# Kernel tuning notes

Measured on AMD Instinct MI355X. Metric: run time of the kernel, lower is better.

The kernel has to match this reference:

```python
import jax, jax.numpy as jnp
import numpy as np

T, A, E, RAW, H, NACT, NTP = 64, 48, 22, 512, 256, 21, 3
# entity_distinct: self entity [0], friendly entities [1:12], hostile entities [12:22]
PARAM_SHAPES = [
    ("W1", (NTP, RAW, H)), ("b1", (NTP, H)), ("W2", (NTP, H, H)), ("b2", (NTP, H)),
    ("WCf", (NTP, 2 * H, H)), ("bCf", (NTP, H)), ("WMf", (NTP, 2 * H + 2 * RAW, H)), ("bMf", (NTP, H)),
    ("WCh", (NTP, 2 * H, H)), ("bCh", (NTP, H)), ("WMh", (NTP, 2 * H + 2 * RAW, H)), ("bMh", (NTP, H)),
    ("L1", (NTP, 2 * H, H)), ("bL1", (NTP, H)), ("L2", (NTP, H, H // 2)), ("bL2", (NTP, H // 2)),
    ("L3", (NTP, H // 2, NACT)), ("bL3", (NTP, NACT)),
    ("V1", (NTP, 2 * H, H)), ("bV1", (NTP, H)), ("V2", (NTP, H, 1)), ("bV2", (NTP, 1)),
]
PNAMES = [n for n, _ in PARAM_SHAPES]


def setup_inputs() -> dict:
    key = jax.random.key(0)
    ks = jax.random.split(key, 3 + len(PARAM_SHAPES))
    inp = {
        "obs": jax.random.normal(ks[0], (T, A, E, RAW), jnp.float32),
        "hete_pick": jax.random.randint(ks[1], (T, A), 0, NTP, jnp.int32),
        "dead": jax.random.bernoulli(ks[2], 0.15, (T, A, E)),
    }
    for i, (n, s) in enumerate(PARAM_SHAPES):
        inp[n] = jax.random.normal(ks[3 + i], s, jnp.float32) * 0.02
    return inp


def _net_forward(p, obs, dead):
    relu = jax.nn.relu
    obs = jnp.where(dead[..., None], 0.0, obs)                    # nan_to_num for dead entities
    v = relu(obs @ p["W1"] + p["b1"]) @ p["W2"] + p["b2"]         # [T,A,E,H] per-entity encoder
    zs, ze_f, ze_h = obs[..., 0, :], obs[..., 1:12, :], obs[..., 12:22, :]
    vs, ve_f, ve_h = v[..., 0, :], v[..., 1:12, :], v[..., 12:22, :]
    df, dh = dead[..., 1:12], dead[..., 12:22]

    def conc(ve, d, ze, WC, bC, WM, bM):
        w = (~d).astype(obs.dtype)                                # alive mask [T,A,Ef]
        denom = jnp.maximum(w.sum(-1, keepdims=True), 1.0)
        pool = jnp.einsum('taeh,tae->tah', ve, w) / denom         # masked mean over entities
        pool_z = jnp.einsum('taer,tae->tar', ze, w) / denom       # skip-connect raw-obs pool
        vC = relu(jnp.concatenate([vs, pool], -1) @ WC + bC)
        vM = relu(jnp.concatenate([vs, pool, zs, pool_z], -1) @ WM + bM)
        return vC, vM

    vfC, vfM = conc(ve_f, df, ze_f, p["WCf"], p["bCf"], p["WMf"], p["bMf"])
    vhC, vhM = conc(ve_h, dh, ze_h, p["WCh"], p["bCh"], p["WMh"], p["bMh"])
    vC = jnp.concatenate([vfC, vhC], -1)                          # [T,A,2H] dual-conc fuse
    vM = jnp.concatenate([vfM, vhM], -1)
    logits = relu(relu(vC @ p["L1"] + p["bL1"]) @ p["L2"] + p["bL2"]) @ p["L3"] + p["bL3"]
    value = relu(vM @ p["V1"] + p["bV1"]) @ p["V2"] + p["bV2"]    # [T,A,1]
    logp = jax.nn.log_softmax(logits, -1)
    act = jnp.argmax(logits, -1)                                  # deterministic (test_mode) action
    alp = jnp.take_along_axis(logp, act[..., None], -1)           # [T,A,1] action log-prob
    return act, value, alp


def reference(obs, hete_pick, dead, W1, b1, W2, b2, WCf, bCf, WMf, bMf, WCh, bCh, WMh, bMh,
              L1, bL1, L2, bL2, L3, bL3, V1, bV1, V2, bV2):
    params = dict(W1=W1, b1=b1, W2=W2, b2=b2, WCf=WCf, bCf=bCf, WMf=WMf, bMf=bMf,
                  WCh=WCh, bCh=bCh, WMh=WMh, bMh=bMh, L1=L1, bL1=bL1, L2=L2, bL2=bL2,
                  L3=L3, bL3=bL3, V1=V1, bV1=bV1, V2=V2, bV2=bV2)
    act = jnp.zeros((T, A), jnp.int32)
    value = jnp.zeros((T, A, 1), obs.dtype)
    alp = jnp.zeros((T, A, 1), obs.dtype)
    for t in range(NTP):                                          # heterogeneous dispatch (distribute_compute)
        pt = {k: v[t] for k, v in params.items()}
        a_t, v_t, lp_t = _net_forward(pt, obs, dead)
        m = hete_pick == t                                        # mask_arr[t]
        act = jnp.where(m, a_t.astype(jnp.int32), act)
        value = jnp.where(m[..., None], v_t, value)
        alp = jnp.where(m[..., None], lp_t, alp)
    return act, value, alp
```

## Files before the change

kernel.cpp:

```cpp
#include <hip/hip_runtime.h>
#include <cstdint>

#define T_ 64
#define A_ 48
#define NP_ 3072
#define E_ 22
#define RAW_ 512
#define H_ 256
#define NACT_ 21
#define NTP_ 3
#define PV_ 3456
#define RV_ 68096
#define NDEAD_ 67584

typedef unsigned short u16;
typedef __attribute__((ext_vector_type(8))) short short8;
typedef __attribute__((ext_vector_type(4))) short short4v;
typedef __attribute__((ext_vector_type(4))) float floatx4;

__device__ __forceinline__ u16 f2bf(float x) {
    unsigned r;
    asm("v_cvt_pk_bf16_f32 %0, %1, %1" : "=v"(r) : "v"(x));
    return (u16)r;
}
__device__ __forceinline__ float bf2f(u16 h) {
    return __uint_as_float(((unsigned)h) << 16);
}

typedef __attribute__((address_space(1))) const void* gp_t;
typedef __attribute__((address_space(3))) void* lp_t;
__device__ __forceinline__ void gload16(const void* g, void* l) {
    __builtin_amdgcn_global_load_lds((gp_t)g, (lp_t)l, 16, 0, 0);
}

__global__ void k_bucket(const unsigned* __restrict__ deadRaw,
                         const int* __restrict__ hete, int* __restrict__ wsI)
{
    __shared__ int fl[2];
    __shared__ int sc[3], cur[3], sps[3], srs[3];
    int tid = threadIdx.x;
    if (tid < 2) fl[tid] = 0;
    if (tid < 3) { sc[tid] = 0; cur[tid] = 0; }
    __syncthreads();
    int ni = 0, nf = 0;
    for (int i = tid; i < 1024; i += 256) {
        unsigned w = deadRaw[i];
        if (w > 1u) ni = 1;
        if (w != 0u && w != 0x3F800000u) nf = 1;
    }
    if (ni) atomicOr(&fl[0], 1);
    if (nf) atomicOr(&fl[1], 1);
    for (int p = tid; p < NP_; p += 256) atomicAdd(&sc[hete[p]], 1);
    __syncthreads();
    if (tid == 0) {
        int c0 = sc[0], c1 = sc[1], c2 = sc[2];
        int p1 = (c0 + 127) & ~127;
        int p2 = p1 + ((c1 + 127) & ~127);
        sps[0] = 0; sps[1] = p1; sps[2] = p2;
        int r1 = (22 * c0 + 127) & ~127;
        int r2 = r1 + ((22 * c1 + 127) & ~127);
        srs[0] = 0; srs[1] = r1; srs[2] = r2;
        wsI[0] = fl[0] ? (fl[1] ? 2 : 1) : 0;
        wsI[1] = c0; wsI[2] = c1; wsI[3] = c2;
        wsI[4] = 0; wsI[5] = p1; wsI[6] = p2;
        wsI[8] = 0; wsI[9] = r1; wsI[10] = r2;
    }
    __syncthreads();
    int* pairIdx = wsI + 16;
    int* prb = pairIdx + PV_;
    for (int pv = tid; pv < PV_; pv += 256) pairIdx[pv] = -1;
    __syncthreads();
    for (int p = tid; p < NP_; p += 256) {
        int t = hete[p];
        int pos = atomicAdd(&cur[t], 1);
        pairIdx[sps[t] + pos] = p;
    }
    for (int pv = tid; pv < PV_; pv += 256) {
        int t = (pv >= sps[1]) + (pv >= sps[2]);
        prb[pv] = srs[t] + 22 * (pv - sps[t]);
    }
}

__global__ void k_deadmask(const void* __restrict__ dead,
                           const int* __restrict__ wsI, float* __restrict__ dm)
{
    int i = blockIdx.x * 256 + threadIdx.x;
    if (i >= NDEAD_) return;
    int mode = wsI[0];
    bool d;
    if (mode == 0)      d = ((const int*)dead)[i] != 0;
    else if (mode == 1) d = ((const float*)dead)[i] != 0.f;
    else                d = ((const unsigned char*)dead)[i] != 0;
    dm[i] = d ? 0.f : 1.f;
}

__global__ void k_rowobs(const int* __restrict__ cnt, const int* __restrict__ ps,
                         const int* __restrict__ rs, const int* __restrict__ pairIdx,
                         const float* __restrict__ dm, int* __restrict__ rowObs)
{
    int rv = blockIdx.x * 256 + threadIdx.x;
    if (rv >= RV_) return;
    int t = (rv >= rs[1]) + (rv >= rs[2]);
    int local = rv - rs[t];
    int out = -1;
    if (local < 22 * cnt[t]) {
        int pl = local / 22;
        int e = local - pl * 22;
        int p = pairIdx[ps[t] + pl];
        if (p >= 0) {
            int oi = p * 22 + e;
            if (dm[oi] != 0.f) out = oi;
        }
    }
    rowObs[rv] = out;
}

struct WCA {
    const float* W[8]; u16* Hi[8]; u16* Lo[8]; int K[8]; int bs[9];
};
__global__ __launch_bounds__(256) void k_wconv(WCA a)
{
    int blk = blockIdx.x;
    int s = 0;
#pragma unroll
    for (int i = 1; i < 8; ++i) if (blk >= a.bs[i]) s = i;
    int lb = blk - a.bs[s];
    int K = a.K[s];
    int K8 = K >> 3;
    int kc = lb % K8;
    int t  = lb / K8;
    int n  = threadIdx.x;
    const float* w = a.W[s] + (long)t * K * 256 + n;
    short8 hv, lv;
#pragma unroll
    for (int j = 0; j < 8; ++j) {
        float x = w[(long)(kc * 8 + j) * 256];
        u16 hh = f2bf(x);
        hv[j] = (short)hh;
        lv[j] = (short)f2bf(x - bf2f(hh));
    }
    long o = ((long)t * 256 + n) * K + kc * 8;
    *(short8*)(a.Hi[s] + o) = hv;
    *(short8*)(a.Lo[s] + o) = lv;
}

struct GD {
    const void* Aa; const void* Ab;
    const u16* Bh; const u16* Bl;
    const float* bias;
    void* Ca; void* Cb;
    long lda; long ldc;
    int K; int coff;
};
struct GA4 { GD d[4]; };

template<int AMODE, bool RELU, int OUTS>
__global__ __launch_bounds__(256) void k_mgemm(
    GA4 ga, const int* __restrict__ rowIdx, const int* __restrict__ starts)
{
    __shared__ short Ah[128 * 32], Al[128 * 32], Bh[128 * 32], Bl[128 * 32];
    const int tid = threadIdx.x;
    const GD d = ga.d[blockIdx.z];
    const long rb = (long)blockIdx.x * 128;
    const int n0 = blockIdx.y * 128;
    const int t = (rb >= starts[0]) + (rb >= starts[1]);
    const int K = d.K;
    const long lda = d.lda;
    const u16* bhT = d.Bh + ((long)t * 256 + n0) * K;
    const u16* blT = d.Bl + ((long)t * 256 + n0) * K;
    const float* biasT = d.bias + (long)t * 256 + n0;

    const int cs = tid & 3;

    const int ar = tid >> 3;
    const int ac = (tid & 7) * 4;
    long arow[4]; float amask[4];
    const float* Afp = (const float*)d.Aa;
    if (AMODE == 1) {
#pragma unroll
        for (int it = 0; it < 4; ++it) {
            int r = 32 * it + ar;
            int i0 = rowIdx[rb + r];
            amask[it] = (i0 < 0) ? 0.f : 1.f;
            arow[it] = (i0 < 0) ? 0 : (long)i0 * lda;
        }
    }
    const u16* ahT = (const u16*)d.Aa;
    const u16* alT = (const u16*)d.Ab;

    const int wave = tid >> 6;
    const int lane = tid & 63;
    const int wr = (wave >> 1) * 64;
    const int wc = (wave & 1) * 64;
    const int lm = lane & 15;
    const int quad = lane >> 4;

    floatx4 acc[4][4];
#pragma unroll
    for (int i = 0; i < 4; ++i)
#pragma unroll
        for (int j = 0; j < 4; ++j) acc[i][j] = (floatx4){0.f, 0.f, 0.f, 0.f};

    for (int k0 = 0; k0 < K; k0 += 32) {
        float4 av[4];
        if (AMODE == 1) {
#pragma unroll
            for (int it = 0; it < 4; ++it)
                av[it] = *(const float4*)(Afp + arow[it] + k0 + ac);
        }
        __syncthreads();
#pragma unroll
        for (int i = 0; i < 2; ++i) {
            int c = i * 256 + tid;
            int r = c >> 2;
            long go = (long)r * K + k0 + ((cs ^ (r & 3)) << 3);
            gload16(bhT + go, &Bh[c << 3]);
            gload16(blT + go, &Bl[c << 3]);
        }
        if (AMODE == 0) {
#pragma unroll
            for (int i = 0; i < 2; ++i) {
                int c = i * 256 + tid;
                int r = c >> 2;
                long go = (rb + r) * lda + k0 + ((cs ^ (r & 3)) << 3);
                gload16(ahT + go, &Ah[c << 3]);
                gload16(alT + go, &Al[c << 3]);
            }
        } else {
#pragma unroll
            for (int it = 0; it < 4; ++it) {
                float xs[4] = {av[it].x, av[it].y, av[it].z, av[it].w};
                short4v hv, lv;
#pragma unroll
                for (int e = 0; e < 4; ++e) {
                    float x = xs[e] * amask[it];
                    u16 hh = f2bf(x);
                    hv[e] = (short)hh;
                    lv[e] = (short)f2bf(x - bf2f(hh));
                }
                int r = 32 * it + ar;
                int bs = ((((ac >> 3) ^ (r & 3))) << 4) | ((ac & 4) << 1);
                *(short4v*)((char*)Ah + r * 64 + bs) = hv;
                *(short4v*)((char*)Al + r * 64 + bs) = lv;
            }
        }
        __syncthreads();
        short8 fah[4], fal[4];
#pragma unroll
        for (int i = 0; i < 4; ++i) {
            int m = wr + 16 * i + lm;
            int sl = (quad ^ (m & 3)) << 3;
            fah[i] = *(const short8*)&Ah[(m << 5) + sl];
            fal[i] = *(const short8*)&Al[(m << 5) + sl];
        }
#pragma unroll
        for (int j = 0; j < 4; ++j) {
            int n = wc + 16 * j + lm;
            int sl = (quad ^ (n & 3)) << 3;
            short8 fbh = *(const short8*)&Bh[(n << 5) + sl];
            short8 fbl = *(const short8*)&Bl[(n << 5) + sl];
#pragma unroll
            for (int i = 0; i < 4; ++i) {
                acc[i][j] = __builtin_amdgcn_mfma_f32_16x16x32_bf16(fah[i], fbh, acc[i][j], 0, 0, 0);
                acc[i][j] = __builtin_amdgcn_mfma_f32_16x16x32_bf16(fal[i], fbh, acc[i][j], 0, 0, 0);
                acc[i][j] = __builtin_amdgcn_mfma_f32_16x16x32_bf16(fah[i], fbl, acc[i][j], 0, 0, 0);
            }
        }
    }
#pragma unroll
    for (int j = 0; j < 4; ++j) {
        int col = wc + 16 * j + lm;
        float bj = biasT[col];
#pragma unroll
        for (int i = 0; i < 4; ++i) {
            long rbase = rb + wr + 16 * i + quad * 4;
#pragma unroll
            for (int r = 0; r < 4; ++r) {
                float vv = acc[i][j][r] + bj;
                if (RELU) vv = fmaxf(vv, 0.f);
                long off = (rbase + r) * d.ldc + d.coff + n0 + col;
                if (OUTS == 0) {
                    ((float*)d.Ca)[off] = vv;
                } else {
                    u16 hh = f2bf(vv);
                    ((u16*)d.Ca)[off] = hh;
                    ((u16*)d.Cb)[off] = f2bf(vv - bf2f(hh));
                }
            }
        }
    }
}

__global__ __launch_bounds__(256) void k_prep(
    const int* __restrict__ pairIdx, const int* __restrict__ prb,
    const float* __restrict__ dm, const float* __restrict__ v,
    const float* __restrict__ obs,
    u16* __restrict__ XFh, u16* __restrict__ XFl,
    u16* __restrict__ XHh, u16* __restrict__ XHl)
{
    int pv = blockIdx.x, c = threadIdx.x;
    int p = pairIdx[pv];
    long xo = (long)pv * 1536;
    if (p < 0) {
        for (int s = 0; s < 6; ++s) {
            XFh[xo + s * 256 + c] = 0; XFl[xo + s * 256 + c] = 0;
            XHh[xo + s * 256 + c] = 0; XHl[xo + s * 256 + c] = 0;
        }
        return;
    }
    __shared__ float sw[22];
    if (c < 22) sw[c] = dm[p * 22 + c];
    __syncthreads();
    float denf = 0.f, denh = 0.f;
    for (int e = 1; e < 12; ++e)  denf += sw[e];
    for (int e = 12; e < 22; ++e) denh += sw[e];
    denf = 1.f / fmaxf(denf, 1.f);
    denh = 1.f / fmaxf(denh, 1.f);

    auto wsp = [&](u16* Hh, u16* Hl, long idx, float val) {
        u16 hh = f2bf(val);
        Hh[idx] = hh;
        Hl[idx] = f2bf(val - bf2f(hh));
    };

    long base = prb[pv];
    float vs = v[base * 256 + c];
    wsp(XFh, XFl, xo + c, vs);
    wsp(XHh, XHl, xo + c, vs);
    float af = 0.f, ah = 0.f;
    for (int e = 1; e < 12; ++e)  af += sw[e] * v[(base + e) * 256 + c];
    for (int e = 12; e < 22; ++e) ah += sw[e] * v[(base + e) * 256 + c];
    wsp(XFh, XFl, xo + 256 + c, af * denf);
    wsp(XHh, XHl, xo + 256 + c, ah * denh);
    const float* ob = obs + (long)p * 22 * 512;
    float w0 = sw[0];
    float z0 = ob[c] * w0;
    float z1 = ob[256 + c] * w0;
    wsp(XFh, XFl, xo + 512 + c, z0); wsp(XHh, XHl, xo + 512 + c, z0);
    wsp(XFh, XFl, xo + 768 + c, z1); wsp(XHh, XHl, xo + 768 + c, z1);
#pragma unroll
    for (int half = 0; half < 2; ++half) {
        int c2 = c + half * 256;
        float zf = 0.f, zh = 0.f;
        for (int e = 1; e < 12; ++e)  zf += sw[e] * ob[(long)e * 512 + c2];
        for (int e = 12; e < 22; ++e) zh += sw[e] * ob[(long)e * 512 + c2];
        wsp(XFh, XFl, xo + 1024 + c2, zf * denf);
        wsp(XHh, XHl, xo + 1024 + c2, zh * denh);
    }
}

__global__ __launch_bounds__(128) void k_final(
    const float* __restrict__ g1, const float* __restrict__ vV,
    const float* __restrict__ L2, const float* __restrict__ bL2,
    const float* __restrict__ L3, const float* __restrict__ bL3,
    const float* __restrict__ V2, const float* __restrict__ bV2,
    const int* __restrict__ pairIdx, const int* __restrict__ ps,
    float* __restrict__ out)
{
    int pv = blockIdx.x;
    int p = pairIdx[pv];
    if (p < 0) return;
    int c = threadIdx.x;
    int t = (pv >= ps[1]) + (pv >= ps[2]);

    __shared__ float sg1[256], sg2[128], sval[2];
    const float* g1p = g1 + (long)pv * 256;
    sg1[c] = g1p[c];
    sg1[c + 128] = g1p[c + 128];

    const float* vv = vV + (long)pv * 256;
    const float* v2t = V2 + t * 256;
    float s = vv[c] * v2t[c] + vv[c + 128] * v2t[c + 128];
    for (int off = 32; off; off >>= 1) s += __shfl_down(s, off);
    if ((c & 63) == 0) sval[c >> 6] = s;
    __syncthreads();

    const float* l2 = L2 + (long)t * 256 * 128 + c;
    float a = bL2[t * 128 + c];
#pragma unroll 8
    for (int k = 0; k < 256; ++k) a = fmaf(sg1[k], l2[(long)k * 128], a);
    sg2[c] = fmaxf(a, 0.f);
    __syncthreads();

    if (c < 64) {
        float lg = -3.0e38f;
        if (c < 21) {
            const float* l3t = L3 + (long)t * 128 * 21 + c;
            float acc = bL3[t * 21 + c];
            for (int k = 0; k < 128; ++k) acc = fmaf(sg2[k], l3t[k * 21], acc);
            lg = acc;
        }
        float mv = lg; int mi = (c < 21) ? c : 9999;
        for (int off = 32; off; off >>= 1) {
            float ov = __shfl_down(mv, off);
            int oi = __shfl_down(mi, off);
            if (ov > mv || (ov == mv && oi < mi)) { mv = ov; mi = oi; }
        }
        mv = __shfl(mv, 0); mi = __shfl(mi, 0);
        float e = (c < 21) ? expf(lg - mv) : 0.f;
        for (int off = 32; off; off >>= 1) e += __shfl_down(e, off);
        if (c == 0) {
            out[p] = (float)mi;
            out[NP_ + p] = sval[0] + sval[1] + bV2[t];
            out[2 * NP_ + p] = -logf(e);
        }
    }
}

extern "C" void kernel_launch(void* const* d_in, const int* in_sizes, int n_in,
                              void* d_out, int out_size, void* d_ws, size_t ws_size,
                              hipStream_t stream)
{
    const float* obs = (const float*)d_in[0];
    const int* hete = (const int*)d_in[1];
    const void* dead = d_in[2];
    const float* W1 = (const float*)d_in[3];  const float* b1 = (const float*)d_in[4];
    const float* W2 = (const float*)d_in[5];  const float* b2 = (const float*)d_in[6];
    const float* WCf = (const float*)d_in[7]; const float* bCf = (const float*)d_in[8];
    const float* WMf = (const float*)d_in[9]; const float* bMf = (const float*)d_in[10];
    const float* WCh = (const float*)d_in[11]; const float* bCh = (const float*)d_in[12];
    const float* WMh = (const float*)d_in[13]; const float* bMh = (const float*)d_in[14];
    const float* L1 = (const float*)d_in[15]; const float* bL1 = (const float*)d_in[16];
    const float* L2 = (const float*)d_in[17]; const float* bL2 = (const float*)d_in[18];
    const float* L3 = (const float*)d_in[19]; const float* bL3 = (const float*)d_in[20];
    const float* V1 = (const float*)d_in[21]; const float* bV1 = (const float*)d_in[22];
    const float* V2 = (const float*)d_in[23]; const float* bV2 = (const float*)d_in[24];
    float* out = (float*)d_out;

    int* wsI = (int*)d_ws;
    int* pairIdx = wsI + 16;
    int* prb = pairIdx + PV_;
    int* rowObs = prb + PV_;
    long fbase = ((16L + PV_ + PV_ + RV_) + 63) & ~63L;
    float* wsF = (float*)d_ws;
    float* dm = wsF + fbase;
    float* cur = dm + NDEAD_;
    auto allocUS = [&](long K) { u16* p = (u16*)cur; cur += (3L * 256 * K) / 2; return p; };
    u16* W1h = allocUS(512);  u16* W1l = allocUS(512);
    u16* W2h = allocUS(256);  u16* W2l = allocUS(256);
    u16* WCfh = allocUS(512); u16* WCfl = allocUS(512);
    u16* WChh = allocUS(512); u16* WChl = allocUS(512);
    u16* WMfh = allocUS(1536); u16* WMfl = allocUS(1536);
    u16* WMhh = allocUS(1536); u16* WMhl = allocUS(1536);
    u16* L1h = allocUS(512);  u16* L1l = allocUS(512);
    u16* V1h = allocUS(512);  u16* V1l = allocUS(512);
    float* regA = cur;
    float* regB = regA + (long)RV_ * 256;

    u16* h1h = (u16*)regA;
    u16* h1l = h1h + (long)RV_ * 256;
    u16* XFh = (u16*)regA;
    u16* XFl = XFh + (long)PV_ * 1536;
    u16* XHh = XFl + (long)PV_ * 1536;
    u16* XHl = XHh + (long)PV_ * 1536;
    float* v = regB;
    u16* vCh = (u16*)regB;
    u16* vCl = vCh + (long)PV_ * 512;
    u16* vMh = vCl + (long)PV_ * 512;
    u16* vMl = vMh + (long)PV_ * 512;
    float* g1 = (float*)(vMl + (long)PV_ * 512);
    float* vV = g1 + (long)PV_ * 256;

    k_bucket<<<1, 256, 0, stream>>>((const unsigned*)dead, hete, wsI);
    k_deadmask<<<264, 256, 0, stream>>>(dead, wsI, dm);
    k_rowobs<<<266, 256, 0, stream>>>(wsI + 1, wsI + 4, wsI + 8, pairIdx, dm, rowObs);

    {
        WCA wa;
        const float* Ws[8] = {W1, W2, WCf, WCh, WMf, WMh, L1, V1};
        u16* His[8] = {W1h, W2h, WCfh, WChh, WMfh, WMhh, L1h, V1h};
        u16* Los[8] = {W1l, W2l, WCfl, WChl, WMfl, WMhl, L1l, V1l};
        int Ks[8] = {512, 256, 512, 512, 1536, 1536, 512, 512};
        int acc_b = 0; wa.bs[0] = 0;
        for (int i = 0; i < 8; ++i) {
            wa.W[i] = Ws[i]; wa.Hi[i] = His[i]; wa.Lo[i] = Los[i]; wa.K[i] = Ks[i];
            acc_b += 3 * Ks[i] / 8; wa.bs[i + 1] = acc_b;
        }
        k_wconv<<<acc_b, 256, 0, stream>>>(wa);
    }

    GA4 g;
    auto setd = [&](int i, const void* Aa, const void* Ab, const u16* Bh_, const u16* Bl_,
                    const float* bias, void* Ca, void* Cb, long lda_, long ldc_, int K_, int coff_) {
        g.d[i] = GD{Aa, Ab, Bh_, Bl_, bias, Ca, Cb, lda_, ldc_, K_, coff_};
    };

    for (int i = 0; i < 4; ++i)
        setd(i, obs, nullptr, W1h, W1l, b1, h1h, h1l, 512, 256, 512, 0);
    k_mgemm<1, true, 1><<<dim3(RV_ / 128, 2, 1), 256, 0, stream>>>(g, rowObs, wsI + 9);

    for (int i = 0; i < 4; ++i)
        setd(i, h1h, h1l, W2h, W2l, b2, v, nullptr, 256, 256, 256, 0);
    k_mgemm<0, false, 0><<<dim3(RV_ / 128, 2, 1), 256, 0, stream>>>(g, nullptr, wsI + 9);

    k_prep<<<PV_, 256, 0, stream>>>(pairIdx, prb, dm, v, obs, XFh, XFl, XHh, XHl);

    setd(0, XFh, XFl, WCfh, WCfl, bCf, vCh, vCl, 1536, 512, 512, 0);
    setd(1, XHh, XHl, WChh, WChl, bCh, vCh, vCl, 1536, 512, 512, 256);
    setd(2, XFh, XFl, WMfh, WMfl, bMf, vMh, vMl, 1536, 512, 1536, 0);
    setd(3, XHh, XHl, WMhh, WMhl, bMh, vMh, vMl, 1536, 512, 1536, 256);
    k_mgemm<0, true, 1><<<dim3(PV_ / 128, 2, 4), 256, 0, stream>>>(g, nullptr, wsI + 5);

    setd(0, vCh, vCl, L1h, L1l, bL1, g1, nullptr, 512, 256, 512, 0);
    setd(1, vMh, vMl, V1h, V1l, bV1, vV, nullptr, 512, 256, 512, 0);
    setd(2, vCh, vCl, L1h, L1l, bL1, g1, nullptr, 512, 256, 512, 0);
    setd(3, vCh, vCl, L1h, L1l, bL1, g1, nullptr, 512, 256, 512, 0);
    k_mgemm<0, true, 0><<<dim3(PV_ / 128, 2, 2), 256, 0, stream>>>(g, nullptr, wsI + 5);

    k_final<<<PV_, 128, 0, stream>>>(g1, vV, L2, bL2, L3, bL3, V2, bV2,
                                     pairIdx, wsI + 4, out);
    (void)in_sizes; (void)n_in; (void)out_size; (void)ws_size;
}
```

Before: 565.2 us.

## Double-buffer GEMM LDS tiles, change swizzle, stage bf16 outputs through LDS

Splits the shared-memory tiles of the split-bf16 grouped GEMM into two buffers. The next K-tile's global-to-LDS loads (and, in the gather mode, its fp32 loads) are issued before the current tile's MFMAs run, so each step needs one barrier instead of two and load latency overlaps compute. The LDS swizzle becomes an XOR of the row bits to cut bank conflicts. The hi/lo bf16 epilogue now writes through LDS so global stores are coalesced 16-byte vectors. LDS use doubles to 64 KB per block, which may lower occupancy.

Measured after the change: 520.3 us. -7.9%, faster.

```diff
diff --git a/kernel.cpp b/kernel.cpp
--- a/kernel.cpp
+++ b/kernel.cpp
@@ -32,6 +32,14 @@
 __device__ __forceinline__ void gload16(const void* g, void* l) {
     __builtin_amdgcn_global_load_lds((gp_t)g, (lp_t)l, 16, 0, 0);
 }
+
+__device__ __forceinline__ void sync_tile() {
+    asm volatile("s_waitcnt vmcnt(0) lgkmcnt(0)" ::: "memory");
+    __builtin_amdgcn_s_barrier();
+    __builtin_amdgcn_sched_barrier(0);
+}
+
+__device__ __forceinline__ int swzk(int r) { return ((r >> 1) ^ r) & 3; }
 
 __global__ void k_bucket(const unsigned* __restrict__ deadRaw,
                          const int* __restrict__ hete, int* __restrict__ wsI)
@@ -158,7 +166,7 @@
 __global__ __launch_bounds__(256) void k_mgemm(
     GA4 ga, const int* __restrict__ rowIdx, const int* __restrict__ starts)
 {
-    __shared__ short Ah[128 * 32], Al[128 * 32], Bh[128 * 32], Bl[128 * 32];
+    __shared__ short smem[32768];
     const int tid = threadIdx.x;
     const GD d = ga.d[blockIdx.z];
     const long rb = (long)blockIdx.x * 128;
@@ -195,68 +203,102 @@
     const int lm = lane & 15;
     const int quad = lane >> 4;
 
-    floatx4 acc[4][4];
-#pragma unroll
-    for (int i = 0; i < 4; ++i)
-#pragma unroll
-        for (int j = 0; j < 4; ++j) acc[i][j] = (floatx4){0.f, 0.f, 0.f, 0.f};
-
-    for (int k0 = 0; k0 < K; k0 += 32) {
-        float4 av[4];
-        if (AMODE == 1) {
-#pragma unroll
-            for (int it = 0; it < 4; ++it)
-                av[it] = *(const float4*)(Afp + arow[it] + k0 + ac);
-        }
-        __syncthreads();
+    auto stageB = [&](int b, int k0) {
+        short* Bh = smem + b * 16384 + 8192;
+        short* Bl = smem + b * 16384 + 12288;
 #pragma unroll
         for (int i = 0; i < 2; ++i) {
             int c = i * 256 + tid;
             int r = c >> 2;
-            long go = (long)r * K + k0 + ((cs ^ (r & 3)) << 3);
+            long go = (long)r * K + k0 + ((cs ^ swzk(r)) << 3);
             gload16(bhT + go, &Bh[c << 3]);
             gload16(blT + go, &Bl[c << 3]);
         }
-        if (AMODE == 0) {
-#pragma unroll
-            for (int i = 0; i < 2; ++i) {
-                int c = i * 256 + tid;
-                int r = c >> 2;
-                long go = (rb + r) * lda + k0 + ((cs ^ (r & 3)) << 3);
-                gload16(ahT + go, &Ah[c << 3]);
-                gload16(alT + go, &Al[c << 3]);
+    };
+    auto stageA0 = [&](int b, int k0) {
+        short* Ah = smem + b * 16384;
+        short* Al = smem + b * 16384 + 4096;
+#pragma unroll
+        for (int i = 0; i < 2; ++i) {
+            int c = i * 256 + tid;
+            int r = c >> 2;
+            long go = (rb + r) * lda + k0 + ((cs ^ swzk(r)) << 3);
+            gload16(ahT + go, &Ah[c << 3]);
+            gload16(alT + go, &Al[c << 3]);
+        }
+    };
+    auto convertA = [&](int b, const float4* av) {
+        short* AhW = smem + b * 16384;
+        short* AlW = AhW + 4096;
+#pragma unroll
+        for (int it = 0; it < 4; ++it) {
+            float xs[4] = {av[it].x, av[it].y, av[it].z, av[it].w};
+            short4v hv, lv;
+#pragma unroll
+            for (int e = 0; e < 4; ++e) {
+                float x = xs[e] * amask[it];
+                u16 hh = f2bf(x);
+                hv[e] = (short)hh;
+                lv[e] = (short)f2bf(x - bf2f(hh));
             }
-        } else {
-#pragma unroll
-            for (int it = 0; it < 4; ++it) {
-                float xs[4] = {av[it].x, av[it].y, av[it].z, av[it].w};
-                short4v hv, lv;
-#pragma unroll
-                for (int e = 0; e < 4; ++e) {
-                    float x = xs[e] * amask[it];
-                    u16 hh = f2bf(x);
-                    hv[e] = (short)hh;
-                    lv[e] = (short)f2bf(x - bf2f(hh));
-                }
-                int r = 32 * it + ar;
-                int bs = ((((ac >> 3) ^ (r & 3))) << 4) | ((ac & 4) << 1);
-                *(short4v*)((char*)Ah + r * 64 + bs) = hv;
-                *(short4v*)((char*)Al + r * 64 + bs) = lv;
+            int r = 32 * it + ar;
+            int bs = (((ac >> 3) ^ swzk(r)) << 4) | ((ac & 4) << 1);
+            *(short4v*)((char*)AhW + r * 64 + bs) = hv;
+            *(short4v*)((char*)AlW + r * 64 + bs) = lv;
+        }
+    };
+
+    floatx4 acc[4][4];
+#pragma unroll
+    for (int i = 0; i < 4; ++i)
+#pragma unroll
+        for (int j = 0; j < 4; ++j) acc[i][j] = (floatx4){0.f, 0.f, 0.f, 0.f};
+
+    if (AMODE == 1) {
+        float4 av0[4];
+#pragma unroll
+        for (int it = 0; it < 4; ++it)
+            av0[it] = *(const float4*)(Afp + arow[it] + ac);
+        stageB(0, 0);
+        convertA(0, av0);
+    } else {
+        stageA0(0, 0);
+        stageB(0, 0);
+    }
+    sync_tile();
+
+    const int nt = K >> 5;
+    int cur = 0;
+    for (int ti = 0; ti < nt; ++ti) {
+        const bool pf = (ti + 1) < nt;
+        const int k1 = (ti + 1) << 5;
+        float4 av2[4];
+        if (pf) {
+            if (AMODE == 1) {
+#pragma unroll
+                for (int it = 0; it < 4; ++it)
+                    av2[it] = *(const float4*)(Afp + arow[it] + k1 + ac);
+            } else {
+                stageA0(cur ^ 1, k1);
             }
-        }
-        __syncthreads();
+            stageB(cur ^ 1, k1);
+        }
+        const short* Ah = smem + cur * 16384;
+        const short* Al = Ah + 4096;
+        const short* Bh = Ah + 8192;
+        const short* Bl = Ah + 12288;
         short8 fah[4], fal[4];
 #pragma unroll
         for (int i = 0; i < 4; ++i) {
             int m = wr + 16 * i + lm;
-            int sl = (quad ^ (m & 3)) << 3;
+            int sl = (quad ^ swzk(m)) << 3;
             fah[i] = *(const short8*)&Ah[(m << 5) + sl];
             fal[i] = *(const short8*)&Al[(m << 5) + sl];
         }
 #pragma unroll
         for (int j = 0; j < 4; ++j) {
             int n = wc + 16 * j + lm;
-            int sl = (quad ^ (n & 3)) << 3;
+            int sl = (quad ^ swzk(n)) << 3;
             short8 fbh = *(const short8*)&Bh[(n << 5) + sl];
             short8 fbl = *(const short8*)&Bl[(n << 5) + sl];
 #pragma unroll
@@ -266,27 +308,66 @@
                 acc[i][j] = __builtin_amdgcn_mfma_f32_16x16x32_bf16(fah[i], fbl, acc[i][j], 0, 0, 0);
             }
         }
-    }
-#pragma unroll
-    for (int j = 0; j < 4; ++j) {
-        int col = wc + 16 * j + lm;
-        float bj = biasT[col];
-#pragma unroll
-        for (int i = 0; i < 4; ++i) {
-            long rbase = rb + wr + 16 * i + quad * 4;
-#pragma unroll
-            for (int r = 0; r < 4; ++r) {
-                float vv = acc[i][j][r] + bj;
-                if (RELU) vv = fmaxf(vv, 0.f);
-                long off = (rbase + r) * d.ldc + d.coff + n0 + col;
-                if (OUTS == 0) {
-                    ((float*)d.Ca)[off] = vv;
-                } else {
-                    u16 hh = f2bf(vv);
-                    ((u16*)d.Ca)[off] = hh;
-                    ((u16*)d.Cb)[off] = f2bf(vv - bf2f(hh));
+        if (pf && AMODE == 1) convertA(cur ^ 1, av2);
+        sync_tile();
+        cur ^= 1;
+    }
+
+    if (OUTS == 0) {
+        float* C = (float*)d.Ca;
+#pragma unroll
+        for (int j = 0; j < 4; ++j) {
+            int col = wc + 16 * j + lm;
+            float bj = biasT[col];
+#pragma unroll
+            for (int i = 0; i < 4; ++i) {
+                long rbase = rb + wr + 16 * i + quad * 4;
+#pragma unroll
+                for (int r = 0; r < 4; ++r) {
+                    float vv = acc[i][j][r] + bj;
+                    if (RELU) vv = fmaxf(vv, 0.f);
+                    C[(rbase + r) * d.ldc + d.coff + n0 + col] = vv;
                 }
             }
+        }
+    } else {
+        u16* Chi = (u16*)smem;
+        u16* Clo = Chi + 16384;
+#pragma unroll
+        for (int j = 0; j < 4; ++j) {
+            int col = wc + 16 * j + lm;
+            float bj = biasT[col];
+#pragma unroll
+            for (int i = 0; i < 4; ++i) {
+                int row0 = wr + 16 * i + quad * 4;
+#pragma unroll
+                for (int r = 0; r < 4; ++r) {
+                    float vv = acc[i][j][r] + bj;
+                    if (RELU) vv = fmaxf(vv, 0.f);
+                    int row = row0 + r;
+                    int cc = col ^ (((row >> 2) & 3) << 4);
+                    u16 hh = f2bf(vv);
+                    Chi[row * 128 + cc] = hh;
+                    Clo[row * 128 + cc] = f2bf(vv - bf2f(hh));
+                }
+            }
+        }
+        asm volatile("s_waitcnt lgkmcnt(0)" ::: "memory");
+        __builtin_amdgcn_s_barrier();
+        __builtin_amdgcn_sched_barrier(0);
+        u16* Ca = (u16*)d.Ca;
+        u16* Cb = (u16*)d.Cb;
+#pragma unroll
+        for (int s = 0; s < 8; ++s) {
+            int ch = s * 256 + tid;
+            int row = ch >> 4;
+            int gcol = (ch & 15) * 8;
+            int lo = row * 128 + (gcol ^ (((row >> 2) & 3) << 4));
+            short8 hv = *(const short8*)&Chi[lo];
+            short8 lv = *(const short8*)&Clo[lo];
+            long go = (rb + row) * d.ldc + d.coff + n0 + gcol;
+            *(short8*)(Ca + go) = hv;
+            *(short8*)(Cb + go) = lv;
         }
     }
 }
```
